# Performance work log

Measured on AMD Instinct MI355X. Metric: run time of the kernel, lower is better.

The kernel has to match this reference:

```python
import jax, jax.numpy as jnp
import numpy as np

V, H, E, L = 50257, 2048, 1024, 4


def setup_inputs() -> dict:
    key = jax.random.key(0)
    ks = jax.random.split(key, 9)
    s = 0.02
    emb = jax.random.normal(ks[0], (V, E), dtype=jnp.float32) * s
    W_ih0 = jax.random.normal(ks[1], (4 * H, E), dtype=jnp.float32) * s   # layer 0 input weights
    W_ihR = jax.random.normal(ks[2], (L - 1, 4 * H, H), dtype=jnp.float32) * s  # layers 1..L-1
    W_hh = jax.random.normal(ks[3], (L, 4 * H, H), dtype=jnp.float32) * s
    b_ih = jax.random.normal(ks[4], (L, 4 * H), dtype=jnp.float32) * s
    b_hh = jax.random.normal(ks[5], (L, 4 * H), dtype=jnp.float32) * s
    fc_W = jax.random.normal(ks[6], (E, H), dtype=jnp.float32) * s
    fc_b = jax.random.normal(ks[7], (E,), dtype=jnp.float32) * s
    inp = jax.random.randint(ks[8], (1,), 0, V, dtype=jnp.int64 if jax.config.jax_enable_x64 else jnp.int32)
    hidden = jnp.zeros((L, 1, H), dtype=jnp.float32)
    cell = jnp.zeros((L, 1, H), dtype=jnp.float32)
    return {"input": inp, "hidden": hidden, "cell": cell, "emb": emb,
            "W_ih0": W_ih0, "W_ihR": W_ihR, "W_hh": W_hh, "b_ih": b_ih,
            "b_hh": b_hh, "fc_W": fc_W, "fc_b": fc_b}


def reference(input, hidden, cell, emb, W_ih0, W_ihR, W_hh, b_ih, b_hh, fc_W, fc_b):
    # embedding lookup: [1, E]
    x = emb[input]
    h_out, c_out = [], []
    for l in range(L):  # small fixed layer loop (structurally distinct weights)
        W_ih = W_ih0 if l == 0 else W_ihR[l - 1]
        gates = x @ W_ih.T + hidden[l] @ W_hh[l].T + b_ih[l] + b_hh[l]  # [1, 4H]
        i, f, g, o = jnp.split(gates, 4, axis=-1)  # torch gate order i,f,g,o
        i, f, o = jax.nn.sigmoid(i), jax.nn.sigmoid(f), jax.nn.sigmoid(o)
        g = jnp.tanh(g)
        c = f * cell[l] + i * g
        h = o * jnp.tanh(c)
        h_out.append(h)
        c_out.append(c)
        x = h
    hidden_new = jnp.stack(h_out, axis=0)  # [L, 1, H]
    cell_new = jnp.stack(c_out, axis=0)
    decoded = x @ fc_W.T + fc_b  # [1, E]
    return decoded, hidden_new, cell_new
```

## Files before the change

### kernel.cpp

```cpp
#include <hip/hip_runtime.h>
#include <math.h>

#define LSTM_H 2048
#define LSTM_E 1024
#define LSTM_L 4
#define FOURH  8192

typedef float f32x4 __attribute__((ext_vector_type(4)));

__device__ __forceinline__ float sigmoidf_(float x) {
    return 1.0f / (1.0f + __expf(-x));
}

__device__ __forceinline__ float wave_reduce(float s) {
    #pragma unroll
    for (int off = 32; off > 0; off >>= 1)
        s += __shfl_down(s, off, 64);
    return s;
}

__device__ __forceinline__ float dot2048(const float* __restrict__ w,
                                         const float* __restrict__ v, int lane) {
    const float4* __restrict__ w4 = (const float4*)w;
    const float4* __restrict__ v4 = (const float4*)v;
    float s = 0.0f;
    #pragma unroll
    for (int t = 0; t < 8; ++t) {
        const int idx = lane + t * 64;
        float4 a = w4[idx];
        float4 b = v4[idx];
        s += a.x * b.x + a.y * b.y + a.z * b.z + a.w * b.w;
    }
    return s;
}

__device__ __forceinline__ float dot1024(const float* __restrict__ w,
                                         const float* __restrict__ v, int lane) {
    const float4* __restrict__ w4 = (const float4*)w;
    const float4* __restrict__ v4 = (const float4*)v;
    float s = 0.0f;
    #pragma unroll
    for (int t = 0; t < 4; ++t) {
        const int idx = lane + t * 64;
        float4 a = w4[idx];
        float4 b = v4[idx];
        s += a.x * b.x + a.y * b.y + a.z * b.z + a.w * b.w;
    }
    return s;
}

__device__ __forceinline__ float dot2048_wnt(const float* __restrict__ w,
                                             const float* __restrict__ v, int lane) {
    const f32x4*  __restrict__ w4 = (const f32x4*)w;
    const float4* __restrict__ v4 = (const float4*)v;
    float s = 0.0f;
    #pragma unroll
    for (int t = 0; t < 8; ++t) {
        const int idx = lane + t * 64;
        f32x4  a = __builtin_nontemporal_load(w4 + idx);
        float4 b = v4[idx];
        s += a.x * b.x + a.y * b.y + a.z * b.z + a.w * b.w;
    }
    return s;
}

__global__ __launch_bounds__(256)
void k1_parallel(const int*   __restrict__ token,
                 const float* __restrict__ hidden,
                 const float* __restrict__ cell,
                 const float* __restrict__ emb,
                 const float* __restrict__ W_ih0,
                 const float* __restrict__ W_hh,
                 const float* __restrict__ b_ih,
                 const float* __restrict__ b_hh,
                 float* __restrict__ h_new,
                 float* __restrict__ c_new,
                 float* __restrict__ part)
{
    const int wave = threadIdx.x >> 6;
    const int lane = threadIdx.x & 63;

    if (blockIdx.x < 2048) {
        const int j   = blockIdx.x;
        const int row = wave * LSTM_H + j;

        const float bias  = b_ih[row] + b_hh[row];
        const float c_in0 = cell[j];
        const float* xemb = emb + (size_t)(*token) * LSTM_E;

        float s = dot1024(W_ih0 + (size_t)row * LSTM_E, xemb, lane)
                + dot2048_wnt(W_hh + (size_t)row * LSTM_H, hidden, lane);
        s = wave_reduce(s);

        __shared__ float gsh[4];
        if (lane == 0) gsh[wave] = s + bias;
        __syncthreads();

        if (threadIdx.x == 0) {
            const float i_ = sigmoidf_(gsh[0]);
            const float f_ = sigmoidf_(gsh[1]);
            const float g_ = tanhf(gsh[2]);
            const float o_ = sigmoidf_(gsh[3]);
            const float c  = f_ * c_in0 + i_ * g_;
            c_new[j] = c;
            h_new[j] = o_ * tanhf(c);
        }
    } else {
        const int r     = (blockIdx.x - 2048) * 4 + wave;
        const int lidx  = r >> 13;
        const int rowin = r & (FOURH - 1);

        const size_t brow = (size_t)(lidx + 1) * FOURH + rowin;
        const float bias = b_ih[brow] + b_hh[brow];

        const float* w = W_hh + (size_t)(lidx + 1) * FOURH * LSTM_H
                               + (size_t)rowin * LSTM_H;
        const float* v = hidden + (size_t)(lidx + 1) * LSTM_H;

        float s = dot2048_wnt(w, v, lane);
        s = wave_reduce(s);
        if (lane == 0) part[r] = s + bias;
    }
}

__global__ __launch_bounds__(256)
void kb_layer(const float* __restrict__ W_ih,
              const float* __restrict__ part_l,
              const float* __restrict__ hx,
              const float* __restrict__ c_in,
              float* __restrict__ h_out,
              float* __restrict__ c_out)
{
    const int j    = blockIdx.x;
    const int wave = threadIdx.x >> 6;
    const int lane = threadIdx.x & 63;
    const int row  = wave * LSTM_H + j;

    const float p      = part_l[row];
    const float c_in_j = c_in[j];

    float s = dot2048(W_ih + (size_t)row * LSTM_H, hx, lane);
    s = wave_reduce(s);

    __shared__ float gsh[4];
    if (lane == 0) gsh[wave] = s + p;
    __syncthreads();

    if (threadIdx.x == 0) {
        const float i_ = sigmoidf_(gsh[0]);
        const float f_ = sigmoidf_(gsh[1]);
        const float g_ = tanhf(gsh[2]);
        const float o_ = sigmoidf_(gsh[3]);
        const float c  = f_ * c_in_j + i_ * g_;
        c_out[j] = c;
        h_out[j] = o_ * tanhf(c);
    }
}

__global__ __launch_bounds__(256)
void kfc(const float* __restrict__ fc_W,
         const float* __restrict__ fc_b,
         const float* __restrict__ h,
         float* __restrict__ out)
{
    const int wave = threadIdx.x >> 6;
    const int lane = threadIdx.x & 63;
    const int r = blockIdx.x * 4 + wave;

    const float b = fc_b[r];
    float s = dot2048(fc_W + (size_t)r * LSTM_H, h, lane);
    s = wave_reduce(s);
    if (lane == 0) out[r] = s + b;
}

extern "C" void kernel_launch(void* const* d_in, const int* in_sizes, int n_in,
                              void* d_out, int out_size, void* d_ws, size_t ws_size,
                              hipStream_t stream) {
    const int*   token  = (const int*)d_in[0];
    const float* hidden = (const float*)d_in[1];
    const float* cell   = (const float*)d_in[2];
    const float* emb    = (const float*)d_in[3];
    const float* W_ih0  = (const float*)d_in[4];
    const float* W_ihR  = (const float*)d_in[5];
    const float* W_hh   = (const float*)d_in[6];
    const float* b_ih   = (const float*)d_in[7];
    const float* b_hh   = (const float*)d_in[8];
    const float* fc_W   = (const float*)d_in[9];
    const float* fc_b   = (const float*)d_in[10];

    float* out     = (float*)d_out;
    float* decoded = out;
    float* h_new   = out + LSTM_E;
    float* c_new   = out + LSTM_E + LSTM_L * LSTM_H;
    float* part    = (float*)d_ws;

    const size_t WIH_STRIDE = (size_t)FOURH * LSTM_H;
    const size_t P_STRIDE   = (size_t)FOURH;

    k1_parallel<<<8192, 256, 0, stream>>>(
        token, hidden, cell, emb, W_ih0, W_hh, b_ih, b_hh,
        h_new, c_new, part);

    for (int l = 1; l < LSTM_L; ++l) {
        kb_layer<<<LSTM_H, 256, 0, stream>>>(
            W_ihR + (size_t)(l - 1) * WIH_STRIDE,
            part  + (size_t)(l - 1) * P_STRIDE,
            h_new + (size_t)(l - 1) * LSTM_H,
            cell  + (size_t)l * LSTM_H,
            h_new + (size_t)l * LSTM_H,
            c_new + (size_t)l * LSTM_H);
    }

    kfc<<<LSTM_E / 4, 256, 0, stream>>>(
        fc_W, fc_b, h_new + (size_t)(LSTM_L - 1) * LSTM_H, decoded);
}
```

Baseline: 86.62 us.

## Process two W_hh rows per wave and keep the last layer's weights cacheable

In the non-layer-0 part of the first kernel, each wave now computes two adjacent W_hh row dot products, sharing each hidden-vector load, and the grid shrinks from 8192 to 5120 blocks. The final 2048 rows, belonging to layer 3, use normal loads instead of nontemporal ones so they may stay in cache. This cuts wave count and hidden-vector reloads and raises memory-level parallelism per wave, at the cost of fewer waves in flight and more registers. The selective cache policy looks like an attempt to exploit cache residency across repeated calls.

After: 88.58 us. +2.3%, slower.

```diff
diff --git a/kernel.cpp b/kernel.cpp
--- a/kernel.cpp
+++ b/kernel.cpp
@@ -106,20 +106,54 @@
             h_new[j] = o_ * tanhf(c);
         }
     } else {
-        const int r     = (blockIdx.x - 2048) * 4 + wave;
-        const int lidx  = r >> 13;
-        const int rowin = r & (FOURH - 1);
-
-        const size_t brow = (size_t)(lidx + 1) * FOURH + rowin;
-        const float bias = b_ih[brow] + b_hh[brow];
-
-        const float* w = W_hh + (size_t)(lidx + 1) * FOURH * LSTM_H
-                               + (size_t)rowin * LSTM_H;
-        const float* v = hidden + (size_t)(lidx + 1) * LSTM_H;
-
-        float s = dot2048_wnt(w, v, lane);
-        s = wave_reduce(s);
-        if (lane == 0) part[r] = s + bias;
+        const int p     = (blockIdx.x - 2048) * 4 + wave;
+        const int r0    = 2 * p;
+        const int lidx  = r0 >> 13;
+        const int rowin = r0 & (FOURH - 1);
+
+        const size_t brow0 = (size_t)(lidx + 1) * FOURH + rowin;
+        const float bias0 = b_ih[brow0]     + b_hh[brow0];
+        const float bias1 = b_ih[brow0 + 1] + b_hh[brow0 + 1];
+
+        const float* w0 = W_hh + (size_t)(lidx + 1) * FOURH * LSTM_H
+                                + (size_t)rowin * LSTM_H;
+        const float* v  = hidden + (size_t)(lidx + 1) * LSTM_H;
+
+        const float4* __restrict__ v4  = (const float4*)v;
+        float s0 = 0.f, s1 = 0.f;
+
+        if (r0 >= 24576 - 2048) {
+            const float4* __restrict__ w40 = (const float4*)w0;
+            const float4* __restrict__ w41 = w40 + (LSTM_H / 4);
+            #pragma unroll
+            for (int t = 0; t < 8; ++t) {
+                const int idx = lane + t * 64;
+                const float4 b  = v4[idx];
+                const float4 a0 = w40[idx];
+                const float4 a1 = w41[idx];
+                s0 += a0.x * b.x + a0.y * b.y + a0.z * b.z + a0.w * b.w;
+                s1 += a1.x * b.x + a1.y * b.y + a1.z * b.z + a1.w * b.w;
+            }
+        } else {
+            const f32x4* __restrict__ w40 = (const f32x4*)w0;
+            const f32x4* __restrict__ w41 = w40 + (LSTM_H / 4);
+            #pragma unroll
+            for (int t = 0; t < 8; ++t) {
+                const int idx = lane + t * 64;
+                const float4 b  = v4[idx];
+                const f32x4  a0 = __builtin_nontemporal_load(w40 + idx);
+                const f32x4  a1 = __builtin_nontemporal_load(w41 + idx);
+                s0 += a0.x * b.x + a0.y * b.y + a0.z * b.z + a0.w * b.w;
+                s1 += a1.x * b.x + a1.y * b.y + a1.z * b.z + a1.w * b.w;
+            }
+        }
+
+        s0 = wave_reduce(s0);
+        s1 = wave_reduce(s1);
+        if (lane == 0) {
+            part[(size_t)lidx * FOURH + rowin]     = s0 + bias0;
+            part[(size_t)lidx * FOURH + rowin + 1] = s1 + bias1;
+        }
     }
 }
 
@@ -197,7 +231,7 @@
     const size_t WIH_STRIDE = (size_t)FOURH * LSTM_H;
     const size_t P_STRIDE   = (size_t)FOURH;
 
-    k1_parallel<<<8192, 256, 0, stream>>>(
+    k1_parallel<<<5120, 256, 0, stream>>>(
         token, hidden, cell, emb, W_ih0, W_hh, b_ih, b_hh,
         h_new, c_new, part);
 
```
